# Kernel optimization log

Measured on AMD Instinct MI355X. Metric: run time of the kernel, lower is better.

The kernel has to match this reference:

```python
import jax, jax.numpy as jnp
import numpy as np

# Segment boundaries from the original hard-coded slices: 13,13,13,9,4 repeated twice
SEG_BOUNDS = [0, 13, 26, 39, 48, 52, 65, 78, 91, 100, 104]


def segmented_log_softmax(x):
    # x: [B, 104]; independent log-softmax over each of the 10 fixed segments
    return jnp.concatenate(
        [jax.nn.log_softmax(x[:, a:b], axis=-1)
         for a, b in zip(SEG_BOUNDS[:-1], SEG_BOUNDS[1:])], axis=-1)


def setup_inputs() -> dict:
    key = jax.random.key(0)
    ks = jax.random.split(key, 8)
    B, H, D = 8192, 2048, 104
    return {
        "line": jax.random.normal(ks[0], (B, D), dtype=jnp.float32),
        "hidden": jax.random.normal(ks[1], (B, H), dtype=jnp.float32),
        "U_w": jax.random.normal(ks[2], (H, H), dtype=jnp.float32) * 0.02,
        "U_b": jax.random.normal(ks[3], (H,), dtype=jnp.float32) * 0.02,
        "W_w": jax.random.normal(ks[4], (H, D), dtype=jnp.float32) * 0.02,
        "W_b": jax.random.normal(ks[5], (H,), dtype=jnp.float32) * 0.02,
        "V_w": jax.random.normal(ks[6], (D, H), dtype=jnp.float32) * 0.02,
        "V_b": jax.random.normal(ks[7], (D,), dtype=jnp.float32) * 0.02,
    }


def reference(line, hidden, U_w, U_b, W_w, W_b, V_w, V_b):
    # h_t = sigmoid(U(hidden) + W(line)); torch Linear: y = x @ W.T + b
    h_t = jax.nn.sigmoid(hidden @ U_w.T + U_b + line @ W_w.T + W_b)  # [B, H]
    pred = h_t @ V_w.T + V_b                                          # [B, 104]
    pred_logsoft = segmented_log_softmax(pred)                        # [B, 104]
    return pred_logsoft, h_t
```

## Files before the change

kernel.cpp:

```cpp
#include <hip/hip_runtime.h>
#include <cstdint>
#include <cstddef>


typedef __bf16 bf16x8 __attribute__((ext_vector_type(8)));
typedef float  f32x4  __attribute__((ext_vector_type(4)));
typedef unsigned short ushort8 __attribute__((ext_vector_type(8)));
typedef float  float4v __attribute__((ext_vector_type(4)));

#define BB 8192
#define HH 2048
#define DD 104

static __device__ __forceinline__ unsigned short f2bf(float f) {
  unsigned u = __float_as_uint(f);
  unsigned r = (u + 0x7FFFu + ((u >> 16) & 1u)) >> 16;
  return (unsigned short)r;
}

#define GLD_LDS(g, l)                                                          \
  __builtin_amdgcn_global_load_lds(                                            \
      (__attribute__((address_space(1))) void*)(g),                            \
      (__attribute__((address_space(3))) void*)(l), 16, 0, 0)

__global__ __launch_bounds__(256) void conv_bf16_kernel(
    const float* __restrict__ hidden, const float* __restrict__ Uw,
    unsigned short* __restrict__ out_hidden, unsigned short* __restrict__ out_U) {
  long long i = ((long long)blockIdx.x * blockDim.x + threadIdx.x) * 8;
  const float* src; unsigned short* dst; long long off;
  if (i < (long long)BB * HH) { src = hidden; dst = out_hidden; off = i; }
  else { src = Uw; dst = out_U; off = i - (long long)BB * HH; }
  float4v a = *(const float4v*)(src + off);
  float4v b = *(const float4v*)(src + off + 4);
  ushort8 o;
  o[0]=f2bf(a[0]); o[1]=f2bf(a[1]); o[2]=f2bf(a[2]); o[3]=f2bf(a[3]);
  o[4]=f2bf(b[0]); o[5]=f2bf(b[1]); o[6]=f2bf(b[2]); o[7]=f2bf(b[3]);
  *(ushort8*)(dst + off) = o;
}

__global__ __launch_bounds__(256) void pad_bf16_kernel(
    const float* __restrict__ line, const float* __restrict__ Ww,
    const float* __restrict__ Vw,
    unsigned short* __restrict__ line_pad, unsigned short* __restrict__ Ww_pad,
    unsigned short* __restrict__ Vw_pad) {
  int i = blockIdx.x * blockDim.x + threadIdx.x;
  const int N1 = BB * 128;
  const int N2 = N1 + HH * 128;
  if (i < N1) {
    int r = i >> 7, c = i & 127;
    line_pad[i] = (c < DD) ? f2bf(line[r * DD + c]) : (unsigned short)0;
  } else if (i < N2) {
    int j = i - N1; int r = j >> 7, c = j & 127;
    Ww_pad[j] = (c < DD) ? f2bf(Ww[r * DD + c]) : (unsigned short)0;
  } else {
    int j = i - N2; int r = j >> 11, c = j & 2047;
    Vw_pad[j] = (r < DD) ? f2bf(Vw[r * 2048 + c]) : (unsigned short)0;
  }
}

template <int J>
static __device__ __forceinline__ void ktile(
    int it, unsigned short* smem, int aoff, int boff,
    const unsigned short* pAh, const unsigned short* pAl,
    const unsigned short* pBu, const unsigned short* pBw,
    unsigned short* dA, unsigned short* dB, f32x4 (&acc)[8][4]) {
  constexpr int BUF  = J;
  constexpr int BUFS = (J + 3) & 3;
  int kbs = it * 128 + J * 32 + 96;
  if (kbs >= 2176) kbs = 2144;
  const unsigned short* ar = smem + BUF * 16384 + aoff;
  const unsigned short* br = smem + BUF * 16384 + boff;
  bf16x8 av[4], bv[4];

#pragma unroll
  for (int mi = 0; mi < 4; ++mi) av[mi] = *(const bf16x8*)(ar + mi * 512);
#pragma unroll
  for (int n = 0; n < 4; ++n) bv[n] = *(const bf16x8*)(br + n * 512);
  if (kbs < 2048) {
    GLD_LDS(pAh + kbs, dA + BUFS * 16384);
    GLD_LDS(pAh + kbs + 128 * 2048, dA + BUFS * 16384 + 4096);
  } else {
    GLD_LDS(pAl + (kbs - 2048), dA + BUFS * 16384);
    GLD_LDS(pAl + (kbs - 2048) + 128 * 128, dA + BUFS * 16384 + 4096);
  }
  __builtin_amdgcn_s_barrier();
  asm volatile("s_waitcnt lgkmcnt(0)" ::: "memory");
  __builtin_amdgcn_s_setprio(1);
#pragma unroll
  for (int mi = 0; mi < 4; ++mi)
#pragma unroll
    for (int n = 0; n < 4; ++n)
      acc[mi][n] = __builtin_amdgcn_mfma_f32_16x16x32_bf16(av[mi], bv[n], acc[mi][n], 0, 0, 0);
  __builtin_amdgcn_s_setprio(0);
  __builtin_amdgcn_s_barrier();

#pragma unroll
  for (int mi = 0; mi < 4; ++mi) av[mi] = *(const bf16x8*)(ar + 2048 + mi * 512);
  if (kbs < 2048) {
    GLD_LDS(pBu + kbs, dB + BUFS * 16384);
    GLD_LDS(pBu + kbs + 128 * 2048, dB + BUFS * 16384 + 4096);
  } else {
    GLD_LDS(pBw + (kbs - 2048), dB + BUFS * 16384);
    GLD_LDS(pBw + (kbs - 2048) + 128 * 128, dB + BUFS * 16384 + 4096);
  }
  __builtin_amdgcn_s_barrier();
  asm volatile("s_waitcnt lgkmcnt(0)" ::: "memory");
  __builtin_amdgcn_s_setprio(1);
#pragma unroll
  for (int mi = 0; mi < 4; ++mi)
#pragma unroll
    for (int n = 0; n < 4; ++n)
      acc[4 + mi][n] = __builtin_amdgcn_mfma_f32_16x16x32_bf16(av[mi], bv[n], acc[4 + mi][n], 0, 0, 0);
  __builtin_amdgcn_s_setprio(0);
  asm volatile("s_waitcnt vmcnt(8)" ::: "memory");
  __builtin_amdgcn_s_barrier();
}

__global__ __launch_bounds__(512, 2) void gemm1_kernel(
    const unsigned short* __restrict__ Ahid,
    const unsigned short* __restrict__ Aline,
    const unsigned short* __restrict__ BU,
    const unsigned short* __restrict__ BW,
    const float* __restrict__ Ub, const float* __restrict__ Wb,
    float* __restrict__ outH, unsigned short* __restrict__ outHbf) {
  __shared__ unsigned short smem[65536];
  const int t = threadIdx.x;
  const int l = t & 63;
  const int wid = t >> 6;
  const int wr = wid >> 2, wc = wid & 3;
  const int bid = blockIdx.x;
  const int wg = (bid & 7) * 32 + (bid >> 3);
  const int brow = (wg >> 3) * 256;
  const int bcol = (wg & 7) * 256;

  const int frow = l & 15;
  const int slot_r = (l >> 4) ^ ((frow >> 1) & 3);
  const int lrow = t >> 2;
  const int sl8 = (((t & 3) ^ ((t >> 3) & 3)) * 8);

  const unsigned short* pAh = Ahid + (size_t)(brow + lrow) * 2048 + sl8;
  const unsigned short* pAl = Aline + (size_t)(brow + lrow) * 128 + sl8;
  const unsigned short* pBu = BU + (size_t)(bcol + lrow) * 2048 + sl8;
  const unsigned short* pBw = BW + (size_t)(bcol + lrow) * 128 + sl8;

  unsigned short* dA = smem + t * 8;
  unsigned short* dB = smem + 8192 + t * 8;

  const int aoff = (wr * 128 + frow) * 32 + slot_r * 8;
  const int boff = 8192 + (wc * 64 + frow) * 32 + slot_r * 8;

  f32x4 acc[8][4] = {};

#pragma unroll
  for (int p = 0; p < 3; ++p) {
    GLD_LDS(pAh + p * 32, dA + p * 16384);
    GLD_LDS(pAh + p * 32 + 128 * 2048, dA + p * 16384 + 4096);
    GLD_LDS(pBu + p * 32, dB + p * 16384);
    GLD_LDS(pBu + p * 32 + 128 * 2048, dB + p * 16384 + 4096);
  }
  asm volatile("s_waitcnt vmcnt(8)" ::: "memory");
  __builtin_amdgcn_s_barrier();

  for (int it = 0; it < 17; ++it) {
    ktile<0>(it, smem, aoff, boff, pAh, pAl, pBu, pBw, dA, dB, acc);
    ktile<1>(it, smem, aoff, boff, pAh, pAl, pBu, pBw, dA, dB, acc);
    ktile<2>(it, smem, aoff, boff, pAh, pAl, pBu, pBw, dA, dB, acc);
    ktile<3>(it, smem, aoff, boff, pAh, pAl, pBu, pBw, dA, dB, acc);
  }
  asm volatile("s_waitcnt vmcnt(0)" ::: "memory");

  const int erow = (l >> 4) * 4;
#pragma unroll
  for (int n = 0; n < 4; ++n) {
    const int col = bcol + wc * 64 + n * 16 + frow;
    const float bias = Ub[col] + Wb[col];
#pragma unroll
    for (int m = 0; m < 8; ++m) {
      const int r0 = brow + wr * 128 + m * 16 + erow;
#pragma unroll
      for (int jj = 0; jj < 4; ++jj) {
        const float v = acc[m][n][jj] + bias;
        const float h = 1.0f / (1.0f + __expf(-v));
        const size_t idx = (size_t)(r0 + jj) * HH + col;
        outH[idx] = h;
        outHbf[idx] = f2bf(h);
      }
    }
  }
}

template <int NM, int NN>
static __device__ __forceinline__ void mfma_step(
    const unsigned short* sA, const unsigned short* sB, int arow0, int brow0,
    int frow, int fk, f32x4 (&acc)[NM][NN]) {
  bf16x8 af[NM], bfr[NN];
#pragma unroll
  for (int m = 0; m < NM; ++m)
    af[m] = *(const bf16x8*)(sA + (arow0 + m * 16 + frow) * 32 + fk);
#pragma unroll
  for (int n = 0; n < NN; ++n)
    bfr[n] = *(const bf16x8*)(sB + (brow0 + n * 16 + frow) * 32 + fk);
#pragma unroll
  for (int m = 0; m < NM; ++m)
#pragma unroll
    for (int n = 0; n < NN; ++n)
      acc[m][n] = __builtin_amdgcn_mfma_f32_16x16x32_bf16(af[m], bfr[n], acc[m][n], 0, 0, 0);
}

__global__ __launch_bounds__(256, 2) void gemm2_kernel(
    const unsigned short* __restrict__ A,
    const unsigned short* __restrict__ Bm,
    const float* __restrict__ Vb,
    float* __restrict__ outLS) {
  __shared__ unsigned short sA[64 * 32];
  __shared__ unsigned short sB[128 * 32];
  __shared__ float pred[64 * 105];
  const int t = threadIdx.x;
  const int l = t & 63;
  const int wid = t >> 6, wr = wid >> 1, wc = wid & 1;
  const int brow = blockIdx.x * 64;
  const int srow = t >> 2, scg = t & 3;
  const int frow = l & 15, fk = (l >> 4) * 8;

  const unsigned short* gA = A + (size_t)(brow + srow) * HH + scg * 8;
  const unsigned short* gB = Bm + (size_t)srow * HH + scg * 8;
  unsigned short* lA = sA + t * 8;
  unsigned short* lB = sB + t * 8;

  f32x4 acc[2][4] = {};
  for (int ks = 0; ks < 64; ++ks) {
    __syncthreads();
    GLD_LDS(gA, lA);
    GLD_LDS(gB, lB);
    GLD_LDS(gB + 64 * HH, lB + 64 * 32);
    gA += 32; gB += 32;
    __syncthreads();
    mfma_step<2, 4>(sA, sB, wr * 32, wc * 64, frow, fk, acc);
  }

#pragma unroll
  for (int n = 0; n < 4; ++n) {
    const int col = wc * 64 + n * 16 + frow;
    if (col < DD) {
      const float vb = Vb[col];
#pragma unroll
      for (int m = 0; m < 2; ++m) {
        const int r0 = wr * 32 + m * 16 + (l >> 4) * 4;
#pragma unroll
        for (int j = 0; j < 4; ++j)
          pred[(r0 + j) * 105 + col] = acc[m][n][j] + vb;
      }
    }
  }
  __syncthreads();

  if (t < 64) {
    const int segb[11] = {0, 13, 26, 39, 48, 52, 65, 78, 91, 100, 104};
    const float* p = pred + t * 105;
    float* o = outLS + (size_t)(brow + t) * DD;
    for (int s = 0; s < 10; ++s) {
      const int a = segb[s], b = segb[s + 1];
      float mx = -3.0e38f;
      for (int c = a; c < b; ++c) mx = fmaxf(mx, p[c]);
      float sum = 0.0f;
      for (int c = a; c < b; ++c) sum += __expf(p[c] - mx);
      const float ls = __logf(sum) + mx;
      for (int c = a; c < b; ++c) o[c] = p[c] - ls;
    }
  }
}

extern "C" void kernel_launch(void* const* d_in, const int* in_sizes, int n_in,
                              void* d_out, int out_size, void* d_ws, size_t ws_size,
                              hipStream_t stream) {
  (void)in_sizes; (void)n_in; (void)out_size; (void)ws_size;
  const float* line   = (const float*)d_in[0];
  const float* hidden = (const float*)d_in[1];
  const float* Uw     = (const float*)d_in[2];
  const float* Ub     = (const float*)d_in[3];
  const float* Ww     = (const float*)d_in[4];
  const float* Wb     = (const float*)d_in[5];
  const float* Vw     = (const float*)d_in[6];
  const float* Vb     = (const float*)d_in[7];

  char* ws = (char*)d_ws;
  unsigned short* hid_bf  = (unsigned short*)(ws);
  unsigned short* U_bf    = (unsigned short*)(ws + 33554432);
  unsigned short* line_bf = (unsigned short*)(ws + 41943040);
  unsigned short* Ww_bf   = (unsigned short*)(ws + 44040192);
  unsigned short* Vw_bf   = (unsigned short*)(ws + 44564480);
  unsigned short* ht_bf   = (unsigned short*)(ws + 45088768);

  float* outLS = (float*)d_out;
  float* outH  = (float*)d_out + (size_t)BB * DD;

  conv_bf16_kernel<<<10240, 256, 0, stream>>>(hidden, Uw, hid_bf, U_bf);
  pad_bf16_kernel<<<6144, 256, 0, stream>>>(line, Ww, Vw, line_bf, Ww_bf, Vw_bf);
  gemm1_kernel<<<256, 512, 0, stream>>>(hid_bf, line_bf, U_bf, Ww_bf, Ub, Wb,
                                        outH, ht_bf);
  gemm2_kernel<<<128, 256, 0, stream>>>(ht_bf, Vw_bf, Vb, outLS);
}
```

Baseline: 135.8 us.

## Restructure gemm1 main loop into double-buffered 64-wide K stages with split A/B fragments

The gemm1 K-loop moves from a 4-buffer, 32-wide-K ring to a 2-buffer scheme with 64-wide K stages (two 32 sub-tiles), and A and B get separate LDS regions. Each wave now keeps all 8 A fragments in registers and streams B in pairs. Global-to-LDS loads are issued between MFMA phases, with vmcnt waits and barriers placed per sub-phase. The aim is fewer LDS reloads of A and a better overlap of loads with MFMAs. The cost is higher register pressure and a shallower prefetch depth.

```diff
diff --git a/kernel.cpp b/kernel.cpp
--- a/kernel.cpp
+++ b/kernel.cpp
@@ -22,6 +22,9 @@
   __builtin_amdgcn_global_load_lds(                                            \
       (__attribute__((address_space(1))) void*)(g),                            \
       (__attribute__((address_space(3))) void*)(l), 16, 0, 0)
+
+#define MEMFENCE asm volatile("" ::: "memory")
+#define MFMA16(a, b, c) __builtin_amdgcn_mfma_f32_16x16x32_bf16((a), (b), (c), 0, 0, 0)
 
 __global__ __launch_bounds__(256) void conv_bf16_kernel(
     const float* __restrict__ hidden, const float* __restrict__ Uw,
@@ -58,62 +61,89 @@
   }
 }
 
-template <int J>
+template <int BUF, bool STAGE, bool TAIL>
 static __device__ __forceinline__ void ktile(
-    int it, unsigned short* smem, int aoff, int boff,
+    int kb_n,
+    unsigned short* smem,
     const unsigned short* pAh, const unsigned short* pAl,
     const unsigned short* pBu, const unsigned short* pBw,
-    unsigned short* dA, unsigned short* dB, f32x4 (&acc)[8][4]) {
-  constexpr int BUF  = J;
-  constexpr int BUFS = (J + 3) & 3;
-  int kbs = it * 128 + J * 32 + 96;
-  if (kbs >= 2176) kbs = 2144;
-  const unsigned short* ar = smem + BUF * 16384 + aoff;
-  const unsigned short* br = smem + BUF * 16384 + boff;
-  bf16x8 av[4], bv[4];
-
-#pragma unroll
-  for (int mi = 0; mi < 4; ++mi) av[mi] = *(const bf16x8*)(ar + mi * 512);
-#pragma unroll
-  for (int n = 0; n < 4; ++n) bv[n] = *(const bf16x8*)(br + n * 512);
-  if (kbs < 2048) {
-    GLD_LDS(pAh + kbs, dA + BUFS * 16384);
-    GLD_LDS(pAh + kbs + 128 * 2048, dA + BUFS * 16384 + 4096);
-  } else {
-    GLD_LDS(pAl + (kbs - 2048), dA + BUFS * 16384);
-    GLD_LDS(pAl + (kbs - 2048) + 128 * 128, dA + BUFS * 16384 + 4096);
-  }
-  __builtin_amdgcn_s_barrier();
-  asm volatile("s_waitcnt lgkmcnt(0)" ::: "memory");
+    unsigned short* dA, unsigned short* dB,
+    int aoffs, int boffs, f32x4 (&acc)[8][4]) {
+  constexpr int SB = BUF ^ 1;
+  const unsigned short* Ab = smem + BUF * 16384;
+  const unsigned short* Bb = smem + 32768 + BUF * 16384;
+  const bool hi = STAGE && (kb_n >= 2048);
+  const unsigned short* sA0 = hi ? pAl + (kb_n - 2048) : pAh + kb_n;
+  const unsigned short* sB0 = hi ? pBw + (kb_n - 2048) : pBu + kb_n;
+  const int rstr = hi ? 128 : 2048;
+  bf16x8 a[8], b0, b1;
+
+#pragma unroll
+  for (int mi = 0; mi < 8; ++mi) a[mi] = *(const bf16x8*)(Ab + aoffs + mi * 512);
+  b0 = *(const bf16x8*)(Bb + boffs);
+  b1 = *(const bf16x8*)(Bb + boffs + 512);
+  if (STAGE) {
+    GLD_LDS(sA0, dA + SB * 16384);
+    GLD_LDS(sA0 + 128 * rstr, dA + SB * 16384 + 4096);
+  }
   __builtin_amdgcn_s_setprio(1);
 #pragma unroll
-  for (int mi = 0; mi < 4; ++mi)
-#pragma unroll
-    for (int n = 0; n < 4; ++n)
-      acc[mi][n] = __builtin_amdgcn_mfma_f32_16x16x32_bf16(av[mi], bv[n], acc[mi][n], 0, 0, 0);
+  for (int mi = 0; mi < 8; ++mi) {
+    acc[mi][0] = MFMA16(a[mi], b0, acc[mi][0]);
+    acc[mi][1] = MFMA16(a[mi], b1, acc[mi][1]);
+  }
   __builtin_amdgcn_s_setprio(0);
-  __builtin_amdgcn_s_barrier();
-
-#pragma unroll
-  for (int mi = 0; mi < 4; ++mi) av[mi] = *(const bf16x8*)(ar + 2048 + mi * 512);
-  if (kbs < 2048) {
-    GLD_LDS(pBu + kbs, dB + BUFS * 16384);
-    GLD_LDS(pBu + kbs + 128 * 2048, dB + BUFS * 16384 + 4096);
-  } else {
-    GLD_LDS(pBw + (kbs - 2048), dB + BUFS * 16384);
-    GLD_LDS(pBw + (kbs - 2048) + 128 * 128, dB + BUFS * 16384 + 4096);
-  }
-  __builtin_amdgcn_s_barrier();
-  asm volatile("s_waitcnt lgkmcnt(0)" ::: "memory");
+  MEMFENCE; __builtin_amdgcn_s_barrier(); MEMFENCE;
+
+  b0 = *(const bf16x8*)(Bb + boffs + 1024);
+  b1 = *(const bf16x8*)(Bb + boffs + 1536);
+  if (STAGE) {
+    GLD_LDS(sB0, dB + SB * 16384);
+    GLD_LDS(sB0 + 128 * rstr, dB + SB * 16384 + 4096);
+  }
   __builtin_amdgcn_s_setprio(1);
 #pragma unroll
-  for (int mi = 0; mi < 4; ++mi)
-#pragma unroll
-    for (int n = 0; n < 4; ++n)
-      acc[4 + mi][n] = __builtin_amdgcn_mfma_f32_16x16x32_bf16(av[mi], bv[n], acc[4 + mi][n], 0, 0, 0);
+  for (int mi = 0; mi < 8; ++mi) {
+    acc[mi][2] = MFMA16(a[mi], b0, acc[mi][2]);
+    acc[mi][3] = MFMA16(a[mi], b1, acc[mi][3]);
+  }
   __builtin_amdgcn_s_setprio(0);
-  asm volatile("s_waitcnt vmcnt(8)" ::: "memory");
-  __builtin_amdgcn_s_barrier();
+  if (TAIL) { asm volatile("s_waitcnt vmcnt(0)" ::: "memory"); }
+  else      { asm volatile("s_waitcnt vmcnt(4)" ::: "memory"); }
+  MEMFENCE; __builtin_amdgcn_s_barrier(); MEMFENCE;
+
+#pragma unroll
+  for (int mi = 0; mi < 8; ++mi) a[mi] = *(const bf16x8*)(Ab + 8192 + aoffs + mi * 512);
+  b0 = *(const bf16x8*)(Bb + 8192 + boffs);
+  b1 = *(const bf16x8*)(Bb + 8192 + boffs + 512);
+  if (STAGE) {
+    GLD_LDS(sA0 + 32, dA + SB * 16384 + 8192);
+    GLD_LDS(sA0 + 32 + 128 * rstr, dA + SB * 16384 + 8192 + 4096);
+  }
+  __builtin_amdgcn_s_setprio(1);
+#pragma unroll
+  for (int mi = 0; mi < 8; ++mi) {
+    acc[mi][0] = MFMA16(a[mi], b0, acc[mi][0]);
+    acc[mi][1] = MFMA16(a[mi], b1, acc[mi][1]);
+  }
+  __builtin_amdgcn_s_setprio(0);
+  MEMFENCE; __builtin_amdgcn_s_barrier(); MEMFENCE;
+
+  b0 = *(const bf16x8*)(Bb + 8192 + boffs + 1024);
+  b1 = *(const bf16x8*)(Bb + 8192 + boffs + 1536);
+  if (STAGE) {
+    GLD_LDS(sB0 + 32, dB + SB * 16384 + 8192);
+    GLD_LDS(sB0 + 32 + 128 * rstr, dB + SB * 16384 + 8192 + 4096);
+  }
+  __builtin_amdgcn_s_setprio(1);
+#pragma unroll
+  for (int mi = 0; mi < 8; ++mi) {
+    acc[mi][2] = MFMA16(a[mi], b0, acc[mi][2]);
+    acc[mi][3] = MFMA16(a[mi], b1, acc[mi][3]);
+  }
+  __builtin_amdgcn_s_setprio(0);
+  if (!TAIL) { asm volatile("s_waitcnt vmcnt(4)" ::: "memory"); }
+  MEMFENCE; __builtin_amdgcn_s_barrier(); MEMFENCE;
 }
 
 __global__ __launch_bounds__(512, 2) void gemm1_kernel(
@@ -128,58 +158,57 @@
   const int l = t & 63;
   const int wid = t >> 6;
   const int wr = wid >> 2, wc = wid & 3;
+
   const int bid = blockIdx.x;
   const int wg = (bid & 7) * 32 + (bid >> 3);
   const int brow = (wg >> 3) * 256;
   const int bcol = (wg & 7) * 256;
 
-  const int frow = l & 15;
-  const int slot_r = (l >> 4) ^ ((frow >> 1) & 3);
-  const int lrow = t >> 2;
-  const int sl8 = (((t & 3) ^ ((t >> 3) & 3)) * 8);
-
-  const unsigned short* pAh = Ahid + (size_t)(brow + lrow) * 2048 + sl8;
-  const unsigned short* pAl = Aline + (size_t)(brow + lrow) * 128 + sl8;
-  const unsigned short* pBu = BU + (size_t)(bcol + lrow) * 2048 + sl8;
-  const unsigned short* pBw = BW + (size_t)(bcol + lrow) * 128 + sl8;
-
+  const int frow = l & 15, lhi = l >> 4;
+  const int slot8 = (lhi ^ ((frow >> 1) & 3)) * 8;
+
+  const int srow = t >> 2;
+  const int scol = (((t & 3) ^ ((t >> 3) & 3)) * 8);
+  const unsigned short* pAh = Ahid + (size_t)(brow + srow) * 2048 + scol;
+  const unsigned short* pAl = Aline + (size_t)(brow + srow) * 128 + scol;
+  const unsigned short* pBu = BU + (size_t)(bcol + srow) * 2048 + scol;
+  const unsigned short* pBw = BW + (size_t)(bcol + srow) * 128 + scol;
   unsigned short* dA = smem + t * 8;
-  unsigned short* dB = smem + 8192 + t * 8;
-
-  const int aoff = (wr * 128 + frow) * 32 + slot_r * 8;
-  const int boff = 8192 + (wc * 64 + frow) * 32 + slot_r * 8;
+  unsigned short* dB = smem + 32768 + t * 8;
+
+  const int aoffs = (wr * 128 + frow) * 32 + slot8;
+  const int boffs = (wc * 64 + frow) * 32 + slot8;
 
   f32x4 acc[8][4] = {};
 
-#pragma unroll
-  for (int p = 0; p < 3; ++p) {
-    GLD_LDS(pAh + p * 32, dA + p * 16384);
-    GLD_LDS(pAh + p * 32 + 128 * 2048, dA + p * 16384 + 4096);
-    GLD_LDS(pBu + p * 32, dB + p * 16384);
-    GLD_LDS(pBu + p * 32 + 128 * 2048, dB + p * 16384 + 4096);
-  }
-  asm volatile("s_waitcnt vmcnt(8)" ::: "memory");
-  __builtin_amdgcn_s_barrier();
-
-  for (int it = 0; it < 17; ++it) {
-    ktile<0>(it, smem, aoff, boff, pAh, pAl, pBu, pBw, dA, dB, acc);
-    ktile<1>(it, smem, aoff, boff, pAh, pAl, pBu, pBw, dA, dB, acc);
-    ktile<2>(it, smem, aoff, boff, pAh, pAl, pBu, pBw, dA, dB, acc);
-    ktile<3>(it, smem, aoff, boff, pAh, pAl, pBu, pBw, dA, dB, acc);
-  }
-  asm volatile("s_waitcnt vmcnt(0)" ::: "memory");
-
-  const int erow = (l >> 4) * 4;
-#pragma unroll
-  for (int n = 0; n < 4; ++n) {
-    const int col = bcol + wc * 64 + n * 16 + frow;
+  GLD_LDS(pAh, dA);
+  GLD_LDS(pAh + 128 * 2048, dA + 4096);
+  GLD_LDS(pBu, dB);
+  GLD_LDS(pBu + 128 * 2048, dB + 4096);
+  GLD_LDS(pAh + 32, dA + 8192);
+  GLD_LDS(pAh + 32 + 128 * 2048, dA + 8192 + 4096);
+  GLD_LDS(pBu + 32, dB + 8192);
+  GLD_LDS(pBu + 32 + 128 * 2048, dB + 8192 + 4096);
+  asm volatile("s_waitcnt vmcnt(4)" ::: "memory");
+  __builtin_amdgcn_s_barrier(); MEMFENCE;
+
+  for (int it = 0; it < 16; ++it) {
+    ktile<0, true, false>((2 * it + 1) * 64, smem, pAh, pAl, pBu, pBw, dA, dB, aoffs, boffs, acc);
+    ktile<1, true, false>((2 * it + 2) * 64, smem, pAh, pAl, pBu, pBw, dA, dB, aoffs, boffs, acc);
+  }
+  ktile<0, true, false>(33 * 64, smem, pAh, pAl, pBu, pBw, dA, dB, aoffs, boffs, acc);
+  ktile<1, false, true>(0, smem, pAh, pAl, pBu, pBw, dA, dB, aoffs, boffs, acc);
+
+#pragma unroll
+  for (int nf = 0; nf < 4; ++nf) {
+    const int col = bcol + wc * 64 + nf * 16 + frow;
     const float bias = Ub[col] + Wb[col];
 #pragma unroll
-    for (int m = 0; m < 8; ++m) {
-      const int r0 = brow + wr * 128 + m * 16 + erow;
+    for (int mi = 0; mi < 8; ++mi) {
+      const int r0 = brow + wr * 128 + mi * 16 + lhi * 4;
 #pragma unroll
       for (int jj = 0; jj < 4; ++jj) {
-        const float v = acc[m][n][jj] + bias;
+        const float v = acc[mi][nf][jj] + bias;
         const float h = 1.0f / (1.0f + __expf(-v));
         const size_t idx = (size_t)(r0 + jj) * HH + col;
         outH[idx] = h;
@@ -204,7 +233,7 @@
   for (int m = 0; m < NM; ++m)
 #pragma unroll
     for (int n = 0; n < NN; ++n)
-      acc[m][n] = __builtin_amdgcn_mfma_f32_16x16x32_bf16(af[m], bfr[n], acc[m][n], 0, 0, 0);
+      acc[m][n] = MFMA16(af[m], bfr[n], acc[m][n]);
 }
 
 __global__ __launch_bounds__(256, 2) void gemm2_kernel(
```

Measured after the change: 134.9 us. No clear change (-0.7%).
